# Kernel optimization log

Hardware: AMD Instinct MI355X
Metric: run time of the kernel (lower is better)

Reference implementation:

```python
import jax, jax.numpy as jnp
import numpy as np

N, M = 4194304, 32

def setup_inputs() -> dict:
    key = jax.random.key(0)
    k1, k2, k3 = jax.random.split(key, 3)
    computed = jax.random.normal(k1, (N, M), dtype=jnp.float32)
    target = jax.random.normal(k2, (N, M), dtype=jnp.float32)
    # penalty for false negatives (per-attribute); module default uses 2.0
    penalty = jnp.full((M,), 2.0, dtype=jnp.float32)
    return {"computed": computed, "target": target, "penalty": penalty}

def reference(computed, target, penalty):
    diff = computed - target  # [N, M]
    # where diff < 0 (false negative): -penalty[j] * diff, else diff unchanged
    loss_elems = jnp.where(diff < 0, -penalty[None, :] * diff, diff)
    n_samples = computed.shape[0]
    return jnp.sum(loss_elems) / n_samples
```

## Files before the change

kernel.cpp:

```cpp
#include <hip/hip_runtime.h>

#define BLOCK 256
#define GRID 2048

__global__ __launch_bounds__(BLOCK) void asym_l1_partial(
    const float4* __restrict__ c4, const float4* __restrict__ t4,
    const float* __restrict__ penalty, float* __restrict__ partials, long n4) {
  __shared__ float pen[32];
  if (threadIdx.x < 32) pen[threadIdx.x] = penalty[threadIdx.x];
  __syncthreads();

  float acc = 0.0f;
  const long stride = (long)gridDim.x * blockDim.x;
  for (long i = (long)blockIdx.x * blockDim.x + threadIdx.x; i < n4; i += stride) {
    float4 cv = c4[i];
    float4 tv = t4[i];
    int col = (int)((i * 4) & 31);
    float d0 = cv.x - tv.x;
    float d1 = cv.y - tv.y;
    float d2 = cv.z - tv.z;
    float d3 = cv.w - tv.w;
    acc += (d0 < 0.0f) ? -pen[col + 0] * d0 : d0;
    acc += (d1 < 0.0f) ? -pen[col + 1] * d1 : d1;
    acc += (d2 < 0.0f) ? -pen[col + 2] * d2 : d2;
    acc += (d3 < 0.0f) ? -pen[col + 3] * d3 : d3;
  }

  #pragma unroll
  for (int off = 32; off > 0; off >>= 1) acc += __shfl_down(acc, off, 64);

  __shared__ float wsum[BLOCK / 64];
  const int lane = threadIdx.x & 63;
  const int wid  = threadIdx.x >> 6;
  if (lane == 0) wsum[wid] = acc;
  __syncthreads();
  if (threadIdx.x == 0) {
    float s = 0.0f;
    #pragma unroll
    for (int w = 0; w < BLOCK / 64; ++w) s += wsum[w];
    partials[blockIdx.x] = s;
  }
}

__global__ __launch_bounds__(BLOCK) void asym_l1_final(
    const float* __restrict__ partials, float* __restrict__ out,
    int nparts, float inv_n) {
  float acc = 0.0f;
  for (int i = threadIdx.x; i < nparts; i += BLOCK) acc += partials[i];

  #pragma unroll
  for (int off = 32; off > 0; off >>= 1) acc += __shfl_down(acc, off, 64);

  __shared__ float wsum[BLOCK / 64];
  const int lane = threadIdx.x & 63;
  const int wid  = threadIdx.x >> 6;
  if (lane == 0) wsum[wid] = acc;
  __syncthreads();
  if (threadIdx.x == 0) {
    float s = 0.0f;
    #pragma unroll
    for (int w = 0; w < BLOCK / 64; ++w) s += wsum[w];
    out[0] = s * inv_n;
  }
}

extern "C" void kernel_launch(void* const* d_in, const int* in_sizes, int n_in,
                              void* d_out, int out_size, void* d_ws, size_t ws_size,
                              hipStream_t stream) {
  const float* computed = (const float*)d_in[0];
  const float* target   = (const float*)d_in[1];
  const float* penalty  = (const float*)d_in[2];
  float* out = (float*)d_out;
  float* partials = (float*)d_ws;

  const long total = (long)in_sizes[0];
  const long n4    = total / 4;
  const long n_samples = total / (long)in_sizes[2];
  const float inv_n = 1.0f / (float)n_samples;

  asym_l1_partial<<<GRID, BLOCK, 0, stream>>>(
      (const float4*)computed, (const float4*)target, penalty, partials, n4);
  asym_l1_final<<<1, BLOCK, 0, stream>>>(partials, out, GRID, inv_n);
}
```

Baseline: 194.9 us.

## Unroll grid-stride loop with nontemporal loads and hoisted per-thread penalty

```diff
diff --git a/kernel.cpp b/kernel.cpp
--- a/kernel.cpp
+++ b/kernel.cpp
@@ -3,28 +3,57 @@
 #define BLOCK 256
 #define GRID 2048
 
+typedef float f32x4 __attribute__((ext_vector_type(4)));
+
+__device__ __forceinline__ f32x4 ntload(const f32x4* p) {
+  return __builtin_nontemporal_load(p);
+}
+
+__device__ __forceinline__ float asym4(f32x4 c, f32x4 t,
+                                       float p0, float p1, float p2, float p3) {
+  float d0 = c[0] - t[0], d1 = c[1] - t[1], d2 = c[2] - t[2], d3 = c[3] - t[3];
+  float e0 = (d0 < 0.0f) ? -p0 * d0 : d0;
+  float e1 = (d1 < 0.0f) ? -p1 * d1 : d1;
+  float e2 = (d2 < 0.0f) ? -p2 * d2 : d2;
+  float e3 = (d3 < 0.0f) ? -p3 * d3 : d3;
+  return (e0 + e1) + (e2 + e3);
+}
+
 __global__ __launch_bounds__(BLOCK) void asym_l1_partial(
-    const float4* __restrict__ c4, const float4* __restrict__ t4,
+    const f32x4* __restrict__ c4, const f32x4* __restrict__ t4,
     const float* __restrict__ penalty, float* __restrict__ partials, long n4) {
   __shared__ float pen[32];
   if (threadIdx.x < 32) pen[threadIdx.x] = penalty[threadIdx.x];
   __syncthreads();
 
-  float acc = 0.0f;
-  const long stride = (long)gridDim.x * blockDim.x;
-  for (long i = (long)blockIdx.x * blockDim.x + threadIdx.x; i < n4; i += stride) {
-    float4 cv = c4[i];
-    float4 tv = t4[i];
-    int col = (int)((i * 4) & 31);
-    float d0 = cv.x - tv.x;
-    float d1 = cv.y - tv.y;
-    float d2 = cv.z - tv.z;
-    float d3 = cv.w - tv.w;
-    acc += (d0 < 0.0f) ? -pen[col + 0] * d0 : d0;
-    acc += (d1 < 0.0f) ? -pen[col + 1] * d1 : d1;
-    acc += (d2 < 0.0f) ? -pen[col + 2] * d2 : d2;
-    acc += (d3 < 0.0f) ? -pen[col + 3] * d3 : d3;
+  const long stride = (long)GRID * BLOCK;
+  const long i0 = (long)blockIdx.x * BLOCK + threadIdx.x;
+
+  const int col = (int)((i0 * 4) & 31);
+  const float p0 = pen[col], p1 = pen[col + 1], p2 = pen[col + 2], p3 = pen[col + 3];
+
+  float a0 = 0.0f, a1 = 0.0f, a2 = 0.0f, a3 = 0.0f;
+  long i = i0;
+
+  for (; i + 3 * stride < n4; i += 4 * stride) {
+    f32x4 c0 = ntload(c4 + i);
+    f32x4 c1 = ntload(c4 + i + stride);
+    f32x4 c2 = ntload(c4 + i + 2 * stride);
+    f32x4 c3 = ntload(c4 + i + 3 * stride);
+    f32x4 t0 = ntload(t4 + i);
+    f32x4 t1 = ntload(t4 + i + stride);
+    f32x4 t2 = ntload(t4 + i + 2 * stride);
+    f32x4 t3 = ntload(t4 + i + 3 * stride);
+    a0 += asym4(c0, t0, p0, p1, p2, p3);
+    a1 += asym4(c1, t1, p0, p1, p2, p3);
+    a2 += asym4(c2, t2, p0, p1, p2, p3);
+    a3 += asym4(c3, t3, p0, p1, p2, p3);
   }
+  for (; i < n4; i += stride) {
+    a0 += asym4(ntload(c4 + i), ntload(t4 + i), p0, p1, p2, p3);
+  }
+
+  float acc = (a0 + a1) + (a2 + a3);
 
   #pragma unroll
   for (int off = 32; off > 0; off >>= 1) acc += __shfl_down(acc, off, 64);
@@ -79,6 +108,6 @@
   const float inv_n = 1.0f / (float)n_samples;
 
   asym_l1_partial<<<GRID, BLOCK, 0, stream>>>(
-      (const float4*)computed, (const float4*)target, penalty, partials, n4);
+      (const f32x4*)computed, (const f32x4*)target, penalty, partials, n4);
   asym_l1_final<<<1, BLOCK, 0, stream>>>(partials, out, GRID, inv_n);
 }
```

New measurement: 219.8 us. +12.8%, slower.
